# Kernel optimization log

Measured on AMD Instinct MI355X. Metric: run time of the kernel, lower is better.

The kernel has to match this reference:

```python
import jax, jax.numpy as jnp
import numpy as np
from jax import lax
from jax.scipy.special import logsumexp

B, T, C = 512, 512, 64


def setup_inputs() -> dict:
    key = jax.random.key(0)
    k1, k2, k3, k4, k5 = jax.random.split(key, 5)
    emissions = jax.random.normal(k1, (B, T, C), dtype=jnp.float32)
    tags = jax.random.randint(k2, (B, T), 0, C, dtype=jnp.int32)
    mask = jnp.ones((B, T), dtype=jnp.int32)
    transitions = jax.random.normal(k3, (C, C), dtype=jnp.float32)
    start_transitions = jax.random.normal(k4, (C,), dtype=jnp.float32)
    end_transitions = jax.random.normal(k5, (C,), dtype=jnp.float32)
    return {"emissions": emissions, "tags": tags, "mask": mask,
            "transitions": transitions, "start_transitions": start_transitions,
            "end_transitions": end_transitions}


def _log_partition(emissions, maskb, transitions, start_transitions, end_transitions):
    # forward algorithm: lp [B,C] carried over T-1 steps
    lp0 = start_transitions[None, :] + emissions[:, 0]  # [B,C]

    def step(lp, xs):
        emit_t, mask_t = xs  # [B,C], [B]
        # score[b,i,j] = lp[b,i] + trans[i,j] + emit[b,j]
        score = lp[:, :, None] + transitions[None, :, :] + emit_t[:, None, :]
        lp_next = logsumexp(score, axis=1)  # [B,C]
        lp = jnp.where(mask_t[:, None], lp_next, lp)
        return lp, None

    xs = (jnp.swapaxes(emissions[:, 1:], 0, 1), jnp.swapaxes(maskb[:, 1:], 0, 1))
    lp, _ = lax.scan(step, lp0, xs)
    return logsumexp(lp + end_transitions[None, :], axis=1)  # [B]


def _joint_score(emissions, tags, mask, maskb, transitions, start_transitions, end_transitions):
    b_idx = jnp.arange(emissions.shape[0])
    score0 = start_transitions[tags[:, 0]] + emissions[b_idx, 0, tags[:, 0]]  # [B]
    trans = transitions[tags[:, :-1], tags[:, 1:]]  # [B,T-1]
    emit = jnp.take_along_axis(emissions, tags[:, :, None], axis=2)[:, :, 0]  # [B,T]
    step_scores = jnp.where(maskb[:, 1:], trans + emit[:, 1:], 0.0)
    last_idx = jnp.sum(mask, axis=1).astype(jnp.int32) - 1
    last_tags = tags[b_idx, last_idx]
    return score0 + jnp.sum(step_scores, axis=1) + end_transitions[last_tags]


def reference(emissions, tags, mask, transitions, start_transitions, end_transitions):
    maskb = mask.astype(bool)
    log_denominator = _log_partition(emissions, maskb, transitions, start_transitions, end_transitions)
    log_numerator = _joint_score(emissions, tags, mask, maskb, transitions, start_transitions, end_transitions)
    return jnp.mean(log_denominator - log_numerator)
```

## Files before the change

kernel.cpp:

```cpp
#include <hip/hip_runtime.h>

#define Bn 512
#define Tn 512
#define Cn 64


template <int CTRL>
__device__ __forceinline__ float fmax_dpp(const float v) {
    const int o = __builtin_amdgcn_update_dpp(__float_as_int(v), __float_as_int(v),
                                              CTRL, 0xF, 0xF, false);
    return fmaxf(v, __int_as_float(o));
}

__device__ __forceinline__ float wave_max64(float v) {
    v = fmax_dpp<0x0B1>(v);
    v = fmax_dpp<0x04E>(v);
    v = fmax_dpp<0x141>(v);
    v = fmax_dpp<0x140>(v);
    v = fmax_dpp<0x142>(v);
    v = fmax_dpp<0x143>(v);
    return __int_as_float(__builtin_amdgcn_readlane(__float_as_int(v), 63));
}

__global__ __launch_bounds__(64) void crf_half_kernel(
    const float* __restrict__ emissions,
    const int*   __restrict__ tags,
    const int*   __restrict__ mask,
    const float* __restrict__ transitions,
    const float* __restrict__ start_t,
    const float* __restrict__ end_t,
    float*       __restrict__ ws_alpha,
    float*       __restrict__ ws_beta,
    float*       __restrict__ ws_lsF,
    float*       __restrict__ ws_lsB,
    float*       __restrict__ ws_num)
{
    const int  blk = blockIdx.x;
    const bool fwd = blk < Bn;
    const int  bt  = blk & (Bn - 1);
    const int  j   = threadIdx.x;

    const float* em  = emissions + (size_t)bt * Tn * Cn + j;
    const float* em0 = emissions + (size_t)bt * Tn * Cn;
    const int*   mk  = mask + bt * Tn;
    const int*   tg  = tags + bt * Tn;

    if (fwd) {
        float nsum = 0.f;
        int   mcnt = 0;
        for (int t = j; t < Tn; t += 64) {
            const int tag_t = tg[t];
            const int m_t   = mk[t];
            mcnt += m_t;
            if (t >= 1 && m_t) {
                const int tag_p = tg[t - 1];
                nsum += transitions[tag_p * Cn + tag_t] + em0[t * Cn + tag_t];
            }
        }
#pragma unroll
        for (int off = 32; off > 0; off >>= 1) {
            nsum += __shfl_xor(nsum, off, 64);
            mcnt += __shfl_xor(mcnt, off, 64);
        }

        float w[Cn];
#pragma unroll
        for (int i = 0; i < Cn; ++i) w[i] = __expf(transitions[i * Cn + j]);

        float lp0 = start_t[j] + em[0];
        const float m0 = wave_max64(lp0);
        float log_scale = m0;
        float a_self = __expf(lp0 - m0);

        float cur_e[4];
        int   cur_m[4];
#pragma unroll
        for (int k = 0; k < 4; ++k) {
            cur_e[k] = em[(size_t)(1 + k) * Cn];
            cur_m[k] = mk[1 + k];
        }

        for (int g = 0; g < 64; ++g) {
            float nxt_e[4];
            int   nxt_m[4];
#pragma unroll
            for (int k = 0; k < 4; ++k) {
                const int t = 4 * g + 5 + k;
                nxt_e[k] = em[(size_t)t * Cn];
                nxt_m[k] = mk[t];
            }
            float ex[4];
#pragma unroll
            for (int k = 0; k < 4; ++k) ex[k] = __expf(cur_e[k]);

#pragma unroll
            for (int k = 0; k < 4; ++k) {
                float au[Cn];
#pragma unroll
                for (int i = 0; i < Cn; ++i)
                    au[i] = __int_as_float(
                        __builtin_amdgcn_readlane(__float_as_int(a_self), i));

                float acc0 = 0.f, acc1 = 0.f, acc2 = 0.f, acc3 = 0.f;
#pragma unroll
                for (int i = 0; i < Cn; i += 4) {
                    acc0 = fmaf(au[i + 0], w[i + 0], acc0);
                    acc1 = fmaf(au[i + 1], w[i + 1], acc1);
                    acc2 = fmaf(au[i + 2], w[i + 2], acc2);
                    acc3 = fmaf(au[i + 3], w[i + 3], acc3);
                }
                float s = ((acc0 + acc1) + (acc2 + acc3)) * ex[k];
                if (!cur_m[k]) s = a_self;
                if (k == 3) {
                    const float mx = wave_max64(s);
                    s *= __builtin_amdgcn_rcpf(mx);
                    log_scale += __logf(mx);
                }
                a_self = s;
            }
#pragma unroll
            for (int k = 0; k < 4; ++k) {
                cur_e[k] = nxt_e[k];
                cur_m[k] = nxt_m[k];
            }
        }

        ws_alpha[bt * Cn + j] = a_self;
        if (j == 0) {
            ws_lsF[bt] = log_scale;
            const int t0 = tg[0];
            const int tl = tg[mcnt - 1];
            ws_num[bt] = start_t[t0] + em0[t0] + nsum + end_t[tl];
        }
    } else {
        float w[Cn];
#pragma unroll
        for (int i = 0; i < Cn; ++i) w[i] = __expf(transitions[j * Cn + i]);

        float lp0 = end_t[j];
        const float m0 = wave_max64(lp0);
        float log_scale = m0;
        float b_self = __expf(lp0 - m0);

        float cur_e[4];
        int   cur_m[4];
#pragma unroll
        for (int k = 0; k < 4; ++k) {
            const int u = Tn - 1 - k;
            cur_e[k] = em[(size_t)u * Cn];
            cur_m[k] = mk[u];
        }

        for (int g = 0; g < 64; ++g) {
            float nxt_e[4];
            int   nxt_m[4];
#pragma unroll
            for (int k = 0; k < 4; ++k) {
                const int u = Tn - 5 - 4 * g - k;
                nxt_e[k] = em[(size_t)u * Cn];
                nxt_m[k] = mk[u];
            }
            float ex[4];
#pragma unroll
            for (int k = 0; k < 4; ++k) ex[k] = __expf(cur_e[k]);

#pragma unroll
            for (int k = 0; k < 4; ++k) {
                const int s_idx = 4 * g + k;
                if (s_idx < Tn / 2 - 1) {
                    const float wv = b_self * ex[k];
                    float au[Cn];
#pragma unroll
                    for (int i = 0; i < Cn; ++i)
                        au[i] = __int_as_float(
                            __builtin_amdgcn_readlane(__float_as_int(wv), i));

                    float acc0 = 0.f, acc1 = 0.f, acc2 = 0.f, acc3 = 0.f;
#pragma unroll
                    for (int i = 0; i < Cn; i += 4) {
                        acc0 = fmaf(au[i + 0], w[i + 0], acc0);
                        acc1 = fmaf(au[i + 1], w[i + 1], acc1);
                        acc2 = fmaf(au[i + 2], w[i + 2], acc2);
                        acc3 = fmaf(au[i + 3], w[i + 3], acc3);
                    }
                    float s = ((acc0 + acc1) + (acc2 + acc3));
                    if (!cur_m[k]) s = b_self;
                    if (k == 3) {
                        const float mx = wave_max64(s);
                        s *= __builtin_amdgcn_rcpf(mx);
                        log_scale += __logf(mx);
                    }
                    b_self = s;
                }
            }
#pragma unroll
            for (int k = 0; k < 4; ++k) {
                cur_e[k] = nxt_e[k];
                cur_m[k] = nxt_m[k];
            }
        }

        ws_beta[bt * Cn + j] = b_self;
        if (j == 0) ws_lsB[bt] = log_scale;
    }
}

__global__ __launch_bounds__(64) void crf_combine_kernel(
    const float* __restrict__ ws_alpha,
    const float* __restrict__ ws_beta,
    const float* __restrict__ ws_lsF,
    const float* __restrict__ ws_lsB,
    const float* __restrict__ ws_num,
    float*       __restrict__ out)
{
    const int bt = blockIdx.x;
    const int j  = threadIdx.x;
    float v = ws_alpha[bt * Cn + j] * ws_beta[bt * Cn + j];
#pragma unroll
    for (int off = 32; off > 0; off >>= 1) v += __shfl_xor(v, off, 64);
    if (j == 0) {
        const float denom = ws_lsF[bt] + ws_lsB[bt] + __logf(v);
        atomicAdd(out, (denom - ws_num[bt]) * (1.0f / Bn));
    }
}

__global__ void crf_zero_kernel(float* out) { out[0] = 0.f; }

extern "C" void kernel_launch(void* const* d_in, const int* in_sizes, int n_in,
                              void* d_out, int out_size, void* d_ws, size_t ws_size,
                              hipStream_t stream)
{
    const float* emissions   = (const float*)d_in[0];
    const int*   tags        = (const int*)d_in[1];
    const int*   mask        = (const int*)d_in[2];
    const float* transitions = (const float*)d_in[3];
    const float* start_t     = (const float*)d_in[4];
    const float* end_t       = (const float*)d_in[5];

    float* ws       = (float*)d_ws;
    float* ws_alpha = ws;
    float* ws_beta  = ws_alpha + Bn * Cn;
    float* ws_lsF   = ws_beta + Bn * Cn;
    float* ws_lsB   = ws_lsF + Bn;
    float* ws_num   = ws_lsB + Bn;

    crf_zero_kernel<<<1, 1, 0, stream>>>((float*)d_out);
    crf_half_kernel<<<2 * Bn, Cn, 0, stream>>>(emissions, tags, mask, transitions,
                                               start_t, end_t,
                                               ws_alpha, ws_beta, ws_lsF, ws_lsB, ws_num);
    crf_combine_kernel<<<Bn, Cn, 0, stream>>>(ws_alpha, ws_beta, ws_lsF, ws_lsB,
                                              ws_num, (float*)d_out);
}
```

Measured before the change: 175.2 us.

## Use packed fp16 dot2 for CRF recurrence and single-block finalize

Stores the exponentiated transition matrix as packed fp16 pairs and packs the state vector into half2 through a DPP lane swap. This halves the readlane broadcasts and the dot-product instructions per step by using v_dot2_f32_f16. To keep values inside fp16 range, it now renormalizes with a wave max every step instead of every fourth step, which adds reduction latency to the serial chain. It also replaces the zero kernel, the per-sequence combine kernel and the atomics with a single 512-thread finalize block, removing one launch.

```diff
diff --git a/kernel.cpp b/kernel.cpp
--- a/kernel.cpp
+++ b/kernel.cpp
@@ -4,12 +4,26 @@
 #define Tn 512
 #define Cn 64
 
+
+typedef __fp16 half2_t __attribute__((ext_vector_type(2)));
+
+__device__ __forceinline__ half2_t int_as_half2(int x) {
+    union { int i; half2_t h; } u; u.i = x; return u.h;
+}
+__device__ __forceinline__ int half2_as_int(half2_t h) {
+    union { int i; half2_t h; } u; u.h = h; return u.i;
+}
 
 template <int CTRL>
 __device__ __forceinline__ float fmax_dpp(const float v) {
     const int o = __builtin_amdgcn_update_dpp(__float_as_int(v), __float_as_int(v),
                                               CTRL, 0xF, 0xF, false);
     return fmaxf(v, __int_as_float(o));
+}
+template <int CTRL>
+__device__ __forceinline__ float mov_dpp(const float v) {
+    return __int_as_float(__builtin_amdgcn_update_dpp(
+        __float_as_int(v), __float_as_int(v), CTRL, 0xF, 0xF, false));
 }
 
 __device__ __forceinline__ float wave_max64(float v) {
@@ -20,6 +34,13 @@
     v = fmax_dpp<0x142>(v);
     v = fmax_dpp<0x143>(v);
     return __int_as_float(__builtin_amdgcn_readlane(__float_as_int(v), 63));
+}
+
+__device__ __forceinline__ int pack_pair_f16(const float s, const bool odd) {
+    const float nb = mov_dpp<0x0B1>(s);
+    const float lo = odd ? nb : s;
+    const float hi = odd ? s  : nb;
+    return half2_as_int(__builtin_amdgcn_cvt_pkrtz(lo, hi));
 }
 
 __global__ __launch_bounds__(64) void crf_half_kernel(
@@ -39,6 +60,7 @@
     const bool fwd = blk < Bn;
     const int  bt  = blk & (Bn - 1);
     const int  j   = threadIdx.x;
+    const bool odd = j & 1;
 
     const float* em  = emissions + (size_t)bt * Tn * Cn + j;
     const float* em0 = emissions + (size_t)bt * Tn * Cn;
@@ -63,14 +85,19 @@
             mcnt += __shfl_xor(mcnt, off, 64);
         }
 
-        float w[Cn];
-#pragma unroll
-        for (int i = 0; i < Cn; ++i) w[i] = __expf(transitions[i * Cn + j]);
+        half2_t w2[32];
+#pragma unroll
+        for (int m = 0; m < 32; ++m) {
+            const float w0 = __expf(transitions[(2 * m) * Cn + j]);
+            const float w1 = __expf(transitions[(2 * m + 1) * Cn + j]);
+            w2[m] = __builtin_amdgcn_cvt_pkrtz(w0, w1);
+        }
 
         float lp0 = start_t[j] + em[0];
         const float m0 = wave_max64(lp0);
         float log_scale = m0;
         float a_self = __expf(lp0 - m0);
+        int   a_pk   = pack_pair_f16(a_self, odd);
 
         float cur_e[4];
         int   cur_m[4];
@@ -95,28 +122,27 @@
 
 #pragma unroll
             for (int k = 0; k < 4; ++k) {
-                float au[Cn];
-#pragma unroll
-                for (int i = 0; i < Cn; ++i)
-                    au[i] = __int_as_float(
-                        __builtin_amdgcn_readlane(__float_as_int(a_self), i));
+                int au[32];
+#pragma unroll
+                for (int m = 0; m < 32; ++m)
+                    au[m] = __builtin_amdgcn_readlane(a_pk, 2 * m);
 
                 float acc0 = 0.f, acc1 = 0.f, acc2 = 0.f, acc3 = 0.f;
 #pragma unroll
-                for (int i = 0; i < Cn; i += 4) {
-                    acc0 = fmaf(au[i + 0], w[i + 0], acc0);
-                    acc1 = fmaf(au[i + 1], w[i + 1], acc1);
-                    acc2 = fmaf(au[i + 2], w[i + 2], acc2);
-                    acc3 = fmaf(au[i + 3], w[i + 3], acc3);
+                for (int m = 0; m < 32; m += 4) {
+                    acc0 = __builtin_amdgcn_fdot2(int_as_half2(au[m + 0]), w2[m + 0], acc0, false);
+                    acc1 = __builtin_amdgcn_fdot2(int_as_half2(au[m + 1]), w2[m + 1], acc1, false);
+                    acc2 = __builtin_amdgcn_fdot2(int_as_half2(au[m + 2]), w2[m + 2], acc2, false);
+                    acc3 = __builtin_amdgcn_fdot2(int_as_half2(au[m + 3]), w2[m + 3], acc3, false);
                 }
                 float s = ((acc0 + acc1) + (acc2 + acc3)) * ex[k];
                 if (!cur_m[k]) s = a_self;
-                if (k == 3) {
-                    const float mx = wave_max64(s);
-                    s *= __builtin_amdgcn_rcpf(mx);
-                    log_scale += __logf(mx);
-                }
+
+                const float mx = wave_max64(s);
+                s *= __builtin_amdgcn_rcpf(mx);
+                log_scale += __logf(mx);
                 a_self = s;
+                a_pk   = pack_pair_f16(s, odd);
             }
 #pragma unroll
             for (int k = 0; k < 4; ++k) {
@@ -133,9 +159,13 @@
             ws_num[bt] = start_t[t0] + em0[t0] + nsum + end_t[tl];
         }
     } else {
-        float w[Cn];
-#pragma unroll
-        for (int i = 0; i < Cn; ++i) w[i] = __expf(transitions[j * Cn + i]);
+        half2_t w2[32];
+#pragma unroll
+        for (int m = 0; m < 32; ++m) {
+            const float w0 = __expf(transitions[j * Cn + 2 * m]);
+            const float w1 = __expf(transitions[j * Cn + 2 * m + 1]);
+            w2[m] = __builtin_amdgcn_cvt_pkrtz(w0, w1);
+        }
 
         float lp0 = end_t[j];
         const float m0 = wave_max64(lp0);
@@ -169,27 +199,26 @@
                 const int s_idx = 4 * g + k;
                 if (s_idx < Tn / 2 - 1) {
                     const float wv = b_self * ex[k];
-                    float au[Cn];
-#pragma unroll
-                    for (int i = 0; i < Cn; ++i)
-                        au[i] = __int_as_float(
-                            __builtin_amdgcn_readlane(__float_as_int(wv), i));
+                    const int  b_pk = pack_pair_f16(wv, odd);
+                    int au[32];
+#pragma unroll
+                    for (int m = 0; m < 32; ++m)
+                        au[m] = __builtin_amdgcn_readlane(b_pk, 2 * m);
 
                     float acc0 = 0.f, acc1 = 0.f, acc2 = 0.f, acc3 = 0.f;
 #pragma unroll
-                    for (int i = 0; i < Cn; i += 4) {
-                        acc0 = fmaf(au[i + 0], w[i + 0], acc0);
-                        acc1 = fmaf(au[i + 1], w[i + 1], acc1);
-                        acc2 = fmaf(au[i + 2], w[i + 2], acc2);
-                        acc3 = fmaf(au[i + 3], w[i + 3], acc3);
+                    for (int m = 0; m < 32; m += 4) {
+                        acc0 = __builtin_amdgcn_fdot2(int_as_half2(au[m + 0]), w2[m + 0], acc0, false);
+                        acc1 = __builtin_amdgcn_fdot2(int_as_half2(au[m + 1]), w2[m + 1], acc1, false);
+                        acc2 = __builtin_amdgcn_fdot2(int_as_half2(au[m + 2]), w2[m + 2], acc2, false);
+                        acc3 = __builtin_amdgcn_fdot2(int_as_half2(au[m + 3]), w2[m + 3], acc3, false);
                     }
                     float s = ((acc0 + acc1) + (acc2 + acc3));
                     if (!cur_m[k]) s = b_self;
-                    if (k == 3) {
-                        const float mx = wave_max64(s);
-                        s *= __builtin_amdgcn_rcpf(mx);
-                        log_scale += __logf(mx);
-                    }
+
+                    const float mx = wave_max64(s);
+                    s *= __builtin_amdgcn_rcpf(mx);
+                    log_scale += __logf(mx);
                     b_self = s;
                 }
             }
@@ -205,7 +234,7 @@
     }
 }
 
-__global__ __launch_bounds__(64) void crf_combine_kernel(
+__global__ __launch_bounds__(512) void crf_finalize_kernel(
     const float* __restrict__ ws_alpha,
     const float* __restrict__ ws_beta,
     const float* __restrict__ ws_lsF,
@@ -213,18 +242,24 @@
     const float* __restrict__ ws_num,
     float*       __restrict__ out)
 {
-    const int bt = blockIdx.x;
-    const int j  = threadIdx.x;
-    float v = ws_alpha[bt * Cn + j] * ws_beta[bt * Cn + j];
+    __shared__ float sh[8];
+    const int b = threadIdx.x;
+    float z = 0.f;
+#pragma unroll
+    for (int i = 0; i < Cn; ++i)
+        z += ws_alpha[b * Cn + i] * ws_beta[b * Cn + i];
+    float v = ws_lsF[b] + ws_lsB[b] + __logf(z) - ws_num[b];
 #pragma unroll
     for (int off = 32; off > 0; off >>= 1) v += __shfl_xor(v, off, 64);
-    if (j == 0) {
-        const float denom = ws_lsF[bt] + ws_lsB[bt] + __logf(v);
-        atomicAdd(out, (denom - ws_num[bt]) * (1.0f / Bn));
+    if ((b & 63) == 0) sh[b >> 6] = v;
+    __syncthreads();
+    if (b == 0) {
+        float s = 0.f;
+#pragma unroll
+        for (int k = 0; k < 8; ++k) s += sh[k];
+        out[0] = s * (1.0f / Bn);
     }
 }
-
-__global__ void crf_zero_kernel(float* out) { out[0] = 0.f; }
 
 extern "C" void kernel_launch(void* const* d_in, const int* in_sizes, int n_in,
                               void* d_out, int out_size, void* d_ws, size_t ws_size,
@@ -244,10 +279,9 @@
     float* ws_lsB   = ws_lsF + Bn;
     float* ws_num   = ws_lsB + Bn;
 
-    crf_zero_kernel<<<1, 1, 0, stream>>>((float*)d_out);
     crf_half_kernel<<<2 * Bn, Cn, 0, stream>>>(emissions, tags, mask, transitions,
                                                start_t, end_t,
                                                ws_alpha, ws_beta, ws_lsF, ws_lsB, ws_num);
-    crf_combine_kernel<<<Bn, Cn, 0, stream>>>(ws_alpha, ws_beta, ws_lsF, ws_lsB,
-                                              ws_num, (float*)d_out);
-}
+    crf_finalize_kernel<<<1, 512, 0, stream>>>(ws_alpha, ws_beta, ws_lsF, ws_lsB,
+                                               ws_num, (float*)d_out);
+}
```

New measurement: 192.7 us. +10.0%, slower.
